# Kernel tuning notes

Measured on AMD Instinct MI355X. Metric: run time of the kernel, lower is better.

Reference implementation:

```python
import jax, jax.numpy as jnp
import numpy as np

TIMESTEPS = 1000
DIFFUSION_SPEED = 0.01
B, N = 4, 2048
E = N * (N - 1) // 2  # strict lower-triangular entries per graph


def _build_Qt():
    # Qt[t-1] = [[1-f, f], [f, 1-f]],  f = 0.5*(1-(1-2s)^t), t = 1..T
    ts = jnp.arange(1, TIMESTEPS + 1, dtype=jnp.float32)
    flip = 0.5 * (1.0 - (1.0 - 2.0 * DIFFUSION_SPEED) ** ts)          # [T]
    row0 = jnp.stack([1.0 - flip, flip], axis=-1)                      # [T,2]
    row1 = jnp.stack([flip, 1.0 - flip], axis=-1)                      # [T,2]
    return jnp.stack([row0, row1], axis=1)                             # [T,2,2]


def setup_inputs() -> dict:
    key = jax.random.key(0)
    k1, k2, k3, k4 = jax.random.split(key, 4)
    adj_start = jax.random.randint(k1, (B, N, N), 0, 2, dtype=jnp.int32)
    t = jax.random.randint(k2, (B,), 0, TIMESTEPS, dtype=jnp.int32)
    u = jax.random.uniform(k3, (B, N, N), dtype=jnp.float32)
    q_approx = jax.random.normal(k4, (B, E), dtype=jnp.float32)
    return {"adj_start": adj_start, "t": t, "u": u, "q_approx": q_approx}


def reference(adj_start, t, u, q_approx):
    Qt = _build_Qt()                                                   # [T,2,2]
    # symmetrize raw adjacency into a binary undirected adjacency
    a = jnp.tril(adj_start, -1)
    adj0 = a + jnp.swapaxes(a, -1, -2)                                 # [B,N,N] in {0,1}

    b_idx = jnp.arange(B)[:, None, None]

    # ---- forward diffusion: sample x_t ~ Categorical(Qt[t][adj0]) ----
    probs = Qt[t][b_idx, adj0]                                         # [B,N,N,2]
    x_t = (u < probs[..., 1]).astype(adj0.dtype)                       # [B,N,N]

    # ---- backward diffusion: q(x_{t-1} | x_t, x_0) ----
    Q_likelihood = Qt[0]                                               # [2,2]
    Q_prior = Qt[t - 1]                                                # [B,2,2] (t=0 wraps, as in torch)
    Q_evidence = Qt[t]                                                 # [B,2,2]

    likelihood = Q_likelihood[x_t]                                     # [B,N,N,2]
    prior = Q_prior[b_idx, adj0]                                       # [B,N,N,2]
    evidence = Q_evidence[b_idx, adj0, x_t]                            # [B,N,N]
    q_backward = likelihood * prior / evidence[..., None]              # [B,N,N,2]

    ti, tj = np.tril_indices(N, -1)                                    # static indices
    q_target = q_backward[:, ti, tj, 1]                                # [B,E]

    # ---- BCE-with-logits loss (mean) ----
    x = q_approx
    loss = jnp.mean(jnp.maximum(x, 0.0) - x * q_target + jnp.log1p(jnp.exp(-jnp.abs(x))))
    return loss
```

## Files before the change

### kernel.cpp

```cpp
#include <hip/hip_runtime.h>
#include <math.h>

#define TIMESTEPS 1000
constexpr int Bc = 4;
constexpr int Nc = 2048;
constexpr int EcI = Nc * (Nc - 1) / 2;
constexpr int EG  = EcI / 4;

typedef float f4v __attribute__((ext_vector_type(4)));

__global__ __launch_bounds__(256) void diff_loss_kernel(
    const int* __restrict__ adj, const int* __restrict__ t,
    const float* __restrict__ u, const float* __restrict__ q,
    double* __restrict__ partials)
{
    __shared__ float tab[Bc][8];
    if (threadIdx.x < Bc) {
        int b = threadIdx.x;
        int tb = t[b];
        float f_t = 0.5f * (1.0f - powf(0.98f, (float)(tb + 1)));
        int tpe = (tb == 0) ? TIMESTEPS : tb;
        float f_p = 0.5f * (1.0f - powf(0.98f, (float)tpe));
        float f0  = 0.5f * (1.0f - 0.98f);
        float omf_t = 1.0f - f_t;
        tab[b][0] = f_t;
        tab[b][1] = omf_t;
        tab[b][2] = f0          * f_p          / omf_t;
        tab[b][3] = (1.0f - f0) * f_p          / f_t;
        tab[b][4] = f0          * (1.0f - f_p) / f_t;
        tab[b][5] = (1.0f - f0) * (1.0f - f_p) / omf_t;
    }
    __syncthreads();

    const int totalEG = Bc * EG;
    const int stride = gridDim.x * blockDim.x;
    double acc = 0.0;
    for (int g = blockIdx.x * blockDim.x + threadIdx.x; g < totalEG; g += stride) {
        int b  = g / EG;
        int e0 = (g - b * EG) << 2;

        float sf = sqrtf((float)(8 * e0 + 1));
        int i = (int)((1.0f + sf) * 0.5f);
        if (i * (i - 1) / 2 > e0)  --i;
        if (i * (i + 1) / 2 <= e0) ++i;
        int j = e0 - i * (i - 1) / 2;

        float p0   = tab[b][0], p1   = tab[b][1];
        float qt00 = tab[b][2], qt01 = tab[b][3];
        float qt10 = tab[b][4], qt11 = tab[b][5];

        const f4v q4 = __builtin_nontemporal_load(
            (const f4v*)(q + b * EcI + e0));
        const float qk[4] = {q4.x, q4.y, q4.z, q4.w};

        int ii = i, jj = j;
        float s = 0.0f;
        #pragma unroll
        for (int k = 0; k < 4; ++k) {
            bool adv = (jj >= ii);
            ii += adv;
            jj = adv ? 0 : jj;
            int base = (b << 22) + (ii << 11) + jj;
            int   a0 = __builtin_nontemporal_load(adj + base);
            float uu = __builtin_nontemporal_load(u + base);
            float ps  = a0 ? p1 : p0;
            bool  x   = (uu < ps);
            float t0  = x ? qt01 : qt00;
            float t1  = x ? qt11 : qt10;
            float qtv = a0 ? t1 : t0;
            float qv  = qk[k];
            s += fmaxf(qv, 0.0f) - qv * qtv + __logf(1.0f + __expf(-fabsf(qv)));
            ++jj;
        }
        acc += (double)s;
    }

    for (int off = 32; off > 0; off >>= 1)
        acc += __shfl_down(acc, off, 64);
    __shared__ double wsum[4];
    int lane = threadIdx.x & 63, wid = threadIdx.x >> 6;
    if (lane == 0) wsum[wid] = acc;
    __syncthreads();
    if (threadIdx.x == 0)
        partials[blockIdx.x] = wsum[0] + wsum[1] + wsum[2] + wsum[3];
}

__global__ __launch_bounds__(256) void final_reduce_kernel(
    const double* __restrict__ partials, int nb, float* __restrict__ out)
{
    double acc = 0.0;
    for (int idx = threadIdx.x; idx < nb; idx += blockDim.x)
        acc += partials[idx];
    for (int off = 32; off > 0; off >>= 1)
        acc += __shfl_down(acc, off, 64);
    __shared__ double wsum[4];
    int lane = threadIdx.x & 63, wid = threadIdx.x >> 6;
    if (lane == 0) wsum[wid] = acc;
    __syncthreads();
    if (threadIdx.x == 0)
        out[0] = (float)((wsum[0] + wsum[1] + wsum[2] + wsum[3]) /
                         ((double)Bc * (double)EcI));
}

extern "C" void kernel_launch(void* const* d_in, const int* in_sizes, int n_in,
                              void* d_out, int out_size, void* d_ws, size_t ws_size,
                              hipStream_t stream) {
    const int*   adj = (const int*)d_in[0];
    const int*   t   = (const int*)d_in[1];
    const float* u   = (const float*)d_in[2];
    const float* q   = (const float*)d_in[3];
    float*  out      = (float*)d_out;
    double* partials = (double*)d_ws;

    const int NB = 2048;
    diff_loss_kernel<<<NB, 256, 0, stream>>>(adj, t, u, q, partials);
    final_reduce_kernel<<<1, 256, 0, stream>>>(partials, NB, out);
}
```

Baseline: 164.8 us.

## Split batches between triangular-gather kernel and full-matrix streaming vector-load kernel

Batches 0-1 keep the original per-element triangular gather. Batches 2-3 go to a new kernel that streams whole rows of adj and u with 128-bit vector loads and masks out the upper triangle. The asm volatile keeps the loads live even for upper-triangle chunks, so those bytes are read too. This probes whether full coalesced streaming beats scattered scalar gathers, at the cost of reading roughly twice the adj/u bytes for the streamed batches and running the two kernels back to back.

```diff
diff --git a/kernel.cpp b/kernel.cpp
--- a/kernel.cpp
+++ b/kernel.cpp
@@ -2,41 +2,43 @@
 #include <math.h>
 
 #define TIMESTEPS 1000
-constexpr int Bc = 4;
-constexpr int Nc = 2048;
+constexpr int Bc  = 4;
+constexpr int Nc  = 2048;
 constexpr int EcI = Nc * (Nc - 1) / 2;
 constexpr int EG  = EcI / 4;
 
+typedef int   i4v __attribute__((ext_vector_type(4)));
 typedef float f4v __attribute__((ext_vector_type(4)));
+typedef float f4u __attribute__((ext_vector_type(4), aligned(4)));
 
-__global__ __launch_bounds__(256) void diff_loss_kernel(
+__device__ __forceinline__ void fill_tab(float* tabrow, int tb) {
+    const float f_t = 0.5f * (1.0f - powf(0.98f, (float)(tb + 1)));
+    const int   tpe = (tb == 0) ? TIMESTEPS : tb;
+    const float f_p = 0.5f * (1.0f - powf(0.98f, (float)tpe));
+    const float f0  = 0.01f;
+    const float omf_t = 1.0f - f_t;
+    tabrow[0] = f_t;
+    tabrow[1] = omf_t;
+    tabrow[2] = f0          * f_p          / omf_t;
+    tabrow[3] = (1.0f - f0) * f_p          / f_t;
+    tabrow[4] = f0          * (1.0f - f_p) / f_t;
+    tabrow[5] = (1.0f - f0) * (1.0f - f_p) / omf_t;
+}
+
+__global__ __launch_bounds__(256) void diff_loss_tri_kernel(
     const int* __restrict__ adj, const int* __restrict__ t,
     const float* __restrict__ u, const float* __restrict__ q,
     double* __restrict__ partials)
 {
-    __shared__ float tab[Bc][8];
-    if (threadIdx.x < Bc) {
-        int b = threadIdx.x;
-        int tb = t[b];
-        float f_t = 0.5f * (1.0f - powf(0.98f, (float)(tb + 1)));
-        int tpe = (tb == 0) ? TIMESTEPS : tb;
-        float f_p = 0.5f * (1.0f - powf(0.98f, (float)tpe));
-        float f0  = 0.5f * (1.0f - 0.98f);
-        float omf_t = 1.0f - f_t;
-        tab[b][0] = f_t;
-        tab[b][1] = omf_t;
-        tab[b][2] = f0          * f_p          / omf_t;
-        tab[b][3] = (1.0f - f0) * f_p          / f_t;
-        tab[b][4] = f0          * (1.0f - f_p) / f_t;
-        tab[b][5] = (1.0f - f0) * (1.0f - f_p) / omf_t;
-    }
+    __shared__ float tab[2][8];
+    if (threadIdx.x < 2) fill_tab(tab[threadIdx.x], t[threadIdx.x]);
     __syncthreads();
 
-    const int totalEG = Bc * EG;
+    const int totalEG = 2 * EG;
     const int stride = gridDim.x * blockDim.x;
     double acc = 0.0;
     for (int g = blockIdx.x * blockDim.x + threadIdx.x; g < totalEG; g += stride) {
-        int b  = g / EG;
+        int b  = (g >= EG) ? 1 : 0;
         int e0 = (g - b * EG) << 2;
 
         float sf = sqrtf((float)(8 * e0 + 1));
@@ -49,8 +51,7 @@
         float qt00 = tab[b][2], qt01 = tab[b][3];
         float qt10 = tab[b][4], qt11 = tab[b][5];
 
-        const f4v q4 = __builtin_nontemporal_load(
-            (const f4v*)(q + b * EcI + e0));
+        const f4v q4 = __builtin_nontemporal_load((const f4v*)(q + b * EcI + e0));
         const float qk[4] = {q4.x, q4.y, q4.z, q4.w};
 
         int ii = i, jj = j;
@@ -85,6 +86,75 @@
         partials[blockIdx.x] = wsum[0] + wsum[1] + wsum[2] + wsum[3];
 }
 
+__global__ __launch_bounds__(256) void diff_loss_stream_kernel(
+    const int* __restrict__ adj, const int* __restrict__ t,
+    const float* __restrict__ u, const float* __restrict__ q,
+    double* __restrict__ partials)
+{
+    __shared__ float tab[2][8];
+    if (threadIdx.x < 2) fill_tab(tab[threadIdx.x], t[2 + threadIdx.x]);
+    __syncthreads();
+
+    const int totalC = 2 * (Nc * Nc / 4);
+    const int stride = gridDim.x * blockDim.x;
+    double acc = 0.0;
+    for (int c = blockIdx.x * blockDim.x + threadIdx.x; c < totalC; c += stride) {
+        const int b2  = c >> 20;
+        const int rem = c & ((Nc * Nc / 4) - 1);
+        const int r   = rem >> 9;
+        const int j0  = (rem & 511) << 2;
+
+        const size_t mbase = ((size_t)(2 + b2) << 22) + ((size_t)r << 11) + j0;
+        const i4v a4 = __builtin_nontemporal_load((const i4v*)(adj + mbase));
+        const f4v u4 = __builtin_nontemporal_load((const f4v*)(u + mbase));
+        asm volatile("" :: "v"(a4[0]), "v"(a4[1]), "v"(a4[2]), "v"(a4[3]),
+                           "v"(u4[0]), "v"(u4[1]), "v"(u4[2]), "v"(u4[3]));
+        if (j0 >= r) continue;
+
+        const float p0   = tab[b2][0], p1   = tab[b2][1];
+        const float qt00 = tab[b2][2], qt01 = tab[b2][3];
+        const float qt10 = tab[b2][4], qt11 = tab[b2][5];
+
+        const int e = ((r * (r - 1)) >> 1) + j0;
+        const float* qb = q + (size_t)(2 + b2) * EcI;
+        float qk[4];
+        if (j0 + 4 <= r) {
+            const f4u q4 = __builtin_nontemporal_load((const f4u*)(qb + e));
+            qk[0] = q4.x; qk[1] = q4.y; qk[2] = q4.z; qk[3] = q4.w;
+        } else {
+            #pragma unroll
+            for (int k = 0; k < 4; ++k)
+                qk[k] = (j0 + k < r) ? __builtin_nontemporal_load(qb + e + k)
+                                     : 0.0f;
+        }
+
+        float s = 0.0f;
+        #pragma unroll
+        for (int k = 0; k < 4; ++k) {
+            const int   a0 = a4[k];
+            const float ps = a0 ? p1 : p0;
+            const bool  x  = u4[k] < ps;
+            const float t0 = x ? qt01 : qt00;
+            const float t1 = x ? qt11 : qt10;
+            const float qtv = a0 ? t1 : t0;
+            const float qv  = qk[k];
+            const float term = fmaxf(qv, 0.0f) - qv * qtv
+                             + __logf(1.0f + __expf(-fabsf(qv)));
+            s += (j0 + k < r) ? term : 0.0f;
+        }
+        acc += (double)s;
+    }
+
+    for (int off = 32; off > 0; off >>= 1)
+        acc += __shfl_down(acc, off, 64);
+    __shared__ double wsum[4];
+    int lane = threadIdx.x & 63, wid = threadIdx.x >> 6;
+    if (lane == 0) wsum[wid] = acc;
+    __syncthreads();
+    if (threadIdx.x == 0)
+        partials[1024 + blockIdx.x] = wsum[0] + wsum[1] + wsum[2] + wsum[3];
+}
+
 __global__ __launch_bounds__(256) void final_reduce_kernel(
     const double* __restrict__ partials, int nb, float* __restrict__ out)
 {
@@ -112,7 +182,7 @@
     float*  out      = (float*)d_out;
     double* partials = (double*)d_ws;
 
-    const int NB = 2048;
-    diff_loss_kernel<<<NB, 256, 0, stream>>>(adj, t, u, q, partials);
-    final_reduce_kernel<<<1, 256, 0, stream>>>(partials, NB, out);
+    diff_loss_tri_kernel   <<<1024, 256, 0, stream>>>(adj, t, u, q, partials);
+    diff_loss_stream_kernel<<<1024, 256, 0, stream>>>(adj, t, u, q, partials);
+    final_reduce_kernel<<<1, 256, 0, stream>>>(partials, 2048, out);
 }
```

Result: slower. 170.7 us (+3.6%).
